# Performance work log

Measured on AMD Instinct MI355X. Metric: run time of the kernel, lower is better.

Reference implementation:

```python
import jax, jax.numpy as jnp
import numpy as np

B, FIN, FOUT, FH2, NMIX, LAT, H, W = 16, 256, 256, 256, 8, 512, 64, 64


def _xavier(key, shape):
    # xavier_normal_ over last-two-ish dims; simple fan-based scale
    fan_in = int(np.prod(shape[1:]))
    fan_out = shape[0]
    s = (2.0 / (fan_in + fan_out)) ** 0.5
    return jax.random.normal(key, shape, jnp.float32) * s


def setup_inputs() -> dict:
    key = jax.random.key(0)
    ks = jax.random.split(key, 12)
    return {
        "x": jax.random.normal(ks[0], (B, FIN, H, W), jnp.float32),
        "lat": jax.random.normal(ks[1], (B, LAT), jnp.float32),
        # mixture kernel banks [n_mix, out_ch, in_ch] (kernel_size=1 squeezed)
        "k_in_mix": _xavier(ks[2], (NMIX, FH2, FIN)),
        "k_mid_mix": _xavier(ks[3], (NMIX, FH2, 2 * FH2)),
        "k_out_mix": _xavier(ks[4], (NMIX, FOUT, 2 * FH2)),
        "k_short_mix": _xavier(ks[5], (NMIX, FOUT, FIN)),
        # mixture bias banks [n_mix, ch]
        "b_in_mix": _xavier(ks[6], (NMIX, FH2)),
        "b_mid_mix": _xavier(ks[7], (NMIX, FH2)),
        "b_out_mix": _xavier(ks[8], (NMIX, FOUT)),
        "b_short_mix": _xavier(ks[9], (NMIX, FOUT)),
        # dyna_mix = nn.Linear(lat_size, n_mix) (lat_factor=0 path)
        "w_dyna": _xavier(ks[10], (NMIX, LAT)),
        "b_dyna": jnp.zeros((NMIX,), jnp.float32),
    }


def _complex_wave(h):
    # doubles channel dim: concat(sin, cos) along channels (per sample)
    return jnp.concatenate([jnp.sin(h), jnp.cos(h)], axis=1)


def reference(x, lat, k_in_mix, k_mid_mix, k_out_mix, k_short_mix,
              b_in_mix, b_mid_mix, b_out_mix, b_short_mix, w_dyna, b_dyna):
    # mixing coefficients per sample: [B, n_mix]
    mix = lat @ w_dyna.T + b_dyna
    # per-sample 1x1 conv kernels via mixture reduction: [B, out, in]
    k_in = jnp.einsum('bm,moi->boi', mix, k_in_mix)
    k_mid = jnp.einsum('bm,moi->boi', mix, k_mid_mix)
    k_out = jnp.einsum('bm,moi->boi', mix, k_out_mix)
    k_short = jnp.einsum('bm,moi->boi', mix, k_short_mix)
    # per-sample biases: [B, ch, 1, 1]
    b_in = (mix @ b_in_mix)[:, :, None, None]
    b_mid = (mix @ b_mid_mix)[:, :, None, None]
    b_out = (mix @ b_out_mix)[:, :, None, None]
    b_short = (mix @ b_short_mix)[:, :, None, None]
    # grouped conv with groups = batch (kernel_size=1) == per-sample matmul
    short = jnp.einsum('boi,bihw->bohw', k_short, x) + b_short
    h = jnp.einsum('boi,bihw->bohw', k_in, x) + b_in            # [B, FH2, H, W]
    h = _complex_wave(h)                                        # [B, 2*FH2, H, W]
    h = jnp.einsum('boi,bihw->bohw', k_mid, h) + b_mid
    h = _complex_wave(h)
    out = jnp.einsum('boi,bihw->bohw', k_out, h) + b_out + short
    return out
```

## Files before the change

kernel.cpp:

```cpp
#include <hip/hip_runtime.h>
#include <stdint.h>

#define B_    16
#define FIN   256
#define FOUT  256
#define FH2   256
#define NMIX  8
#define LAT   512
#define HW    4096
#define MT    32

typedef short bf16x8 __attribute__((ext_vector_type(8)));
typedef float f32x4  __attribute__((ext_vector_type(4)));

#define WS_MIX    0
#define WS_BIAS   1024
#define WS_WIN    131072
#define WS_WMID   2228224
#define WS_WOUT   6422528
#define WS_WSHORT 10616832

__device__ __forceinline__ uint16_t f2bf(float f) {
  uint32_t u = __builtin_bit_cast(uint32_t, f);
  u += 0x7fffu + ((u >> 16) & 1u);
  return (uint16_t)(u >> 16);
}
__device__ __forceinline__ uint32_t pack2(float lo, float hi) {
  return (uint32_t)f2bf(lo) | ((uint32_t)f2bf(hi) << 16);
}

#define MFMA(a, b, c) __builtin_amdgcn_mfma_f32_16x16x32_bf16(a, b, c, 0, 0, 0)

__global__ void k_mix_bias(const float* __restrict__ lat,
                           const float* __restrict__ w_dyna,
                           const float* __restrict__ b_dyna,
                           const float* __restrict__ b_in_mix,
                           const float* __restrict__ b_mid_mix,
                           const float* __restrict__ b_out_mix,
                           const float* __restrict__ b_short_mix,
                           float* __restrict__ ws_mix,
                           float* __restrict__ ws_bias) {
  __shared__ float smix[NMIX];
  const int t = threadIdx.x;
  const int lane = t & 63, wv = t >> 6;
  const int b = blockIdx.x;
#pragma unroll
  for (int d2 = 0; d2 < 2; d2++) {
    int m = wv * 2 + d2;
    float s = 0.f;
#pragma unroll
    for (int j = 0; j < 8; j++)
      s += lat[b * LAT + j * 64 + lane] * w_dyna[m * LAT + j * 64 + lane];
#pragma unroll
    for (int off = 32; off; off >>= 1) s += __shfl_xor(s, off);
    if (lane == 0) {
      float v = s + b_dyna[m];
      ws_mix[b * NMIX + m] = v;
      smix[m] = v;
    }
  }
  __syncthreads();
  const float* banks[4] = {b_in_mix, b_mid_mix, b_out_mix, b_short_mix};
  for (int pos = t; pos < 1024; pos += 256) {
    int bank = pos >> 8, ch = pos & 255;
    const float* bp = banks[bank];
    float a = 0.f;
#pragma unroll
    for (int m = 0; m < NMIX; m++) a += smix[m] * bp[m * 256 + ch];
    ws_bias[(bank * B_ + b) * 256 + ch] = a;
  }
}

__global__ void k_weights(const float* __restrict__ k_in_mix,
                          const float* __restrict__ k_mid_mix,
                          const float* __restrict__ k_out_mix,
                          const float* __restrict__ k_short_mix,
                          const float* __restrict__ ws_mix,
                          uint16_t* __restrict__ w_in,
                          uint16_t* __restrict__ w_mid,
                          uint16_t* __restrict__ w_out,
                          uint16_t* __restrict__ w_short) {
  __shared__ float smix[B_ * NMIX];
  const int t = threadIdx.x;
  if (t < B_ * NMIX) smix[t] = ws_mix[t];
  __syncthreads();
  const int idx = blockIdx.x * 256 + t;
  const float* src;
  uint16_t* dst;
  int sstride, dstride;
  if (idx < 65536) {
    int e = idx;
    int j = e & 7, lane = (e >> 3) & 63, ots = (e >> 9) & 3, kt = (e >> 11) & 7, wv = e >> 14;
    int row = wv * 64 + ots * 16 + (lane & 15);
    int k = kt * 32 + (lane >> 4) * 8 + j;
    src = k_in_mix + row * 256 + k; sstride = 65536;
    dst = w_in + e;                 dstride = 65536;
  } else if (idx < 196608) {
    int e = idx - 65536;
    int j = e & 7, lane = (e >> 3) & 63, ots = (e >> 9) & 3, kt = (e >> 11) & 15, wv = e >> 15;
    int row = wv * 64 + ots * 16 + (lane & 15);
    int kp = kt * 32 + (lane >> 4) * 8 + j;
    int i = (kp >> 1) + ((kp & 1) << 8);
    src = k_mid_mix + row * 512 + i; sstride = 131072;
    dst = w_mid + e;                 dstride = 131072;
  } else if (idx < 327680) {
    int e = idx - 196608;
    int j = e & 7, lane = (e >> 3) & 63, ots = (e >> 9) & 3, kt = (e >> 11) & 15, wv = e >> 15;
    int row = wv * 64 + ots * 16 + (lane & 15);
    int kp = kt * 32 + (lane >> 4) * 8 + j;
    int i = (kp >> 1) + ((kp & 1) << 8);
    src = k_out_mix + row * 512 + i; sstride = 131072;
    dst = w_out + e;                 dstride = 131072;
  } else {
    int e = idx - 327680;
    int j = e & 7, lane = (e >> 3) & 63, ots = (e >> 9) & 3, kt = (e >> 11) & 7, wv = e >> 14;
    int row = wv * 64 + ots * 16 + (lane & 15);
    int k = kt * 32 + (lane >> 4) * 8 + j;
    src = k_short_mix + row * 256 + k; sstride = 65536;
    dst = w_short + e;                 dstride = 65536;
  }
  float v[NMIX];
#pragma unroll
  for (int m = 0; m < NMIX; m++) v[m] = src[m * sstride];
  for (int b = 0; b < B_; b++) {
    float a = 0.f;
#pragma unroll
    for (int m = 0; m < NMIX; m++) a += smix[b * NMIX + m] * v[m];
    dst[b * dstride] = f2bf(a);
  }
}

__launch_bounds__(256, 3)
__global__ void k_main(const float* __restrict__ x,
                       const float* __restrict__ ws_bias,
                       const uint16_t* __restrict__ w_in,
                       const uint16_t* __restrict__ w_mid,
                       const uint16_t* __restrict__ w_out,
                       const uint16_t* __restrict__ w_short,
                       float* __restrict__ out) {
  __shared__ int4 smem4[49152 / 16];
  char* lds = (char*)smem4;
  char* Xb = lds;
  char* H1 = lds + 16384;
  char* H2 = lds;

  const int t = threadIdx.x;
  const int lane = t & 63;
  const int wv = t >> 6;
  const int q = lane >> 4;
  const int n = lane & 15;
  const int b = blockIdx.x & 15;
  const int p0 = (blockIdx.x >> 4) * MT;

  {
    const float* xb = x + (size_t)b * FIN * HW + p0;
    const int p = t & 31;
    const int cg = t >> 5;
#pragma unroll
    for (int cc = 0; cc < 4; cc++) {
      int c = cg * 4 + cc;
      float v[8];
#pragma unroll
      for (int e = 0; e < 8; e++) v[e] = xb[(size_t)(c * 8 + e) * HW + p];
      int4 pkt = make_int4((int)pack2(v[0], v[1]), (int)pack2(v[2], v[3]),
                           (int)pack2(v[4], v[5]), (int)pack2(v[6], v[7]));
      *(int4*)(Xb + p * 512 + ((c ^ (p & 7)) * 16)) = pkt;
    }
  }
  __syncthreads();

  f32x4 acc_h[4][2], acc_s[4][2];
#pragma unroll
  for (int ots = 0; ots < 4; ots++) {
    int o = wv * 64 + ots * 16 + q * 4;
    float4 vi = *(const float4*)&ws_bias[(0 * B_ + b) * 256 + o];
    float4 vs = *(const float4*)&ws_bias[(3 * B_ + b) * 256 + o];
    acc_h[ots][0][0] = vi.x; acc_h[ots][0][1] = vi.y; acc_h[ots][0][2] = vi.z; acc_h[ots][0][3] = vi.w;
    acc_h[ots][1] = acc_h[ots][0];
    acc_s[ots][0][0] = vs.x; acc_s[ots][0][1] = vs.y; acc_s[ots][0][2] = vs.z; acc_s[ots][0][3] = vs.w;
    acc_s[ots][1] = acc_s[ots][0];
  }
  {
    const uint16_t* Wi = w_in + (size_t)b * 65536 + wv * 16384 + lane * 8;
    const uint16_t* Ws = w_short + (size_t)b * 65536 + wv * 16384 + lane * 8;
#pragma unroll
    for (int kt = 0; kt < 8; kt++) {
      int sw = ((kt * 4 + q) ^ (n & 7)) * 16;
      bf16x8 bf0 = *(const bf16x8*)(Xb + n * 512 + sw);
      bf16x8 bf1 = *(const bf16x8*)(Xb + (16 + n) * 512 + sw);
#pragma unroll
      for (int ots = 0; ots < 4; ots++) {
        bf16x8 ai = *(const bf16x8*)(Wi + kt * 2048 + ots * 512);
        bf16x8 as = *(const bf16x8*)(Ws + kt * 2048 + ots * 512);
        acc_h[ots][0] = MFMA(ai, bf0, acc_h[ots][0]);
        acc_h[ots][1] = MFMA(ai, bf1, acc_h[ots][1]);
        acc_s[ots][0] = MFMA(as, bf0, acc_s[ots][0]);
        acc_s[ots][1] = MFMA(as, bf1, acc_s[ots][1]);
      }
    }
  }
#pragma unroll
  for (int ots = 0; ots < 4; ots++) {
    int ctile = (wv * 4 + ots) * 4 + q;
#pragma unroll
    for (int pt = 0; pt < 2; pt++) {
      int p = pt * 16 + n;
      uint32_t u0 = pack2(__sinf(acc_h[ots][pt][0]), __cosf(acc_h[ots][pt][0]));
      uint32_t u1 = pack2(__sinf(acc_h[ots][pt][1]), __cosf(acc_h[ots][pt][1]));
      uint32_t u2 = pack2(__sinf(acc_h[ots][pt][2]), __cosf(acc_h[ots][pt][2]));
      uint32_t u3 = pack2(__sinf(acc_h[ots][pt][3]), __cosf(acc_h[ots][pt][3]));
      *(int4*)(H1 + p * 1024 + ((ctile ^ (p & 7)) * 16)) =
          make_int4((int)u0, (int)u1, (int)u2, (int)u3);
    }
  }
  __syncthreads();

  f32x4 acc2[4][2];
#pragma unroll
  for (int ots = 0; ots < 4; ots++) {
    int o = wv * 64 + ots * 16 + q * 4;
    float4 v = *(const float4*)&ws_bias[(1 * B_ + b) * 256 + o];
    acc2[ots][0][0] = v.x; acc2[ots][0][1] = v.y; acc2[ots][0][2] = v.z; acc2[ots][0][3] = v.w;
    acc2[ots][1] = acc2[ots][0];
  }
  {
    const uint16_t* Wm = w_mid + (size_t)b * 131072 + wv * 32768 + lane * 8;
#pragma unroll
    for (int kt = 0; kt < 16; kt++) {
      int sw = ((kt * 4 + q) ^ (n & 7)) * 16;
      bf16x8 bf0 = *(const bf16x8*)(H1 + n * 1024 + sw);
      bf16x8 bf1 = *(const bf16x8*)(H1 + (16 + n) * 1024 + sw);
#pragma unroll
      for (int ots = 0; ots < 4; ots++) {
        bf16x8 am = *(const bf16x8*)(Wm + kt * 2048 + ots * 512);
        acc2[ots][0] = MFMA(am, bf0, acc2[ots][0]);
        acc2[ots][1] = MFMA(am, bf1, acc2[ots][1]);
      }
    }
  }
  __syncthreads();
#pragma unroll
  for (int ots = 0; ots < 4; ots++) {
    int ctile = (wv * 4 + ots) * 4 + q;
#pragma unroll
    for (int pt = 0; pt < 2; pt++) {
      int p = pt * 16 + n;
      uint32_t u0 = pack2(__sinf(acc2[ots][pt][0]), __cosf(acc2[ots][pt][0]));
      uint32_t u1 = pack2(__sinf(acc2[ots][pt][1]), __cosf(acc2[ots][pt][1]));
      uint32_t u2 = pack2(__sinf(acc2[ots][pt][2]), __cosf(acc2[ots][pt][2]));
      uint32_t u3 = pack2(__sinf(acc2[ots][pt][3]), __cosf(acc2[ots][pt][3]));
      *(int4*)(H2 + p * 1024 + ((ctile ^ (p & 7)) * 16)) =
          make_int4((int)u0, (int)u1, (int)u2, (int)u3);
    }
  }
  __syncthreads();

  f32x4 acc3[4][2];
#pragma unroll
  for (int ots = 0; ots < 4; ots++) {
    int o = wv * 64 + ots * 16 + q * 4;
    float4 v = *(const float4*)&ws_bias[(2 * B_ + b) * 256 + o];
    acc3[ots][0][0] = acc_s[ots][0][0] + v.x; acc3[ots][0][1] = acc_s[ots][0][1] + v.y;
    acc3[ots][0][2] = acc_s[ots][0][2] + v.z; acc3[ots][0][3] = acc_s[ots][0][3] + v.w;
    acc3[ots][1][0] = acc_s[ots][1][0] + v.x; acc3[ots][1][1] = acc_s[ots][1][1] + v.y;
    acc3[ots][1][2] = acc_s[ots][1][2] + v.z; acc3[ots][1][3] = acc_s[ots][1][3] + v.w;
  }
  {
    const uint16_t* Wo = w_out + (size_t)b * 131072 + wv * 32768 + lane * 8;
#pragma unroll
    for (int kt = 0; kt < 16; kt++) {
      int sw = ((kt * 4 + q) ^ (n & 7)) * 16;
      bf16x8 bf0 = *(const bf16x8*)(H2 + n * 1024 + sw);
      bf16x8 bf1 = *(const bf16x8*)(H2 + (16 + n) * 1024 + sw);
#pragma unroll
      for (int ots = 0; ots < 4; ots++) {
        bf16x8 ao = *(const bf16x8*)(Wo + kt * 2048 + ots * 512);
        acc3[ots][0] = MFMA(ao, bf0, acc3[ots][0]);
        acc3[ots][1] = MFMA(ao, bf1, acc3[ots][1]);
      }
    }
  }
  {
    float* ob = out + (size_t)b * FOUT * HW + p0;
#pragma unroll
    for (int ots = 0; ots < 4; ots++) {
#pragma unroll
      for (int pt = 0; pt < 2; pt++) {
#pragma unroll
        for (int r = 0; r < 4; r++) {
          int o = wv * 64 + ots * 16 + q * 4 + r;
          ob[(size_t)o * HW + pt * 16 + n] = acc3[ots][pt][r];
        }
      }
    }
  }
}

extern "C" void kernel_launch(void* const* d_in, const int* in_sizes, int n_in,
                              void* d_out, int out_size, void* d_ws, size_t ws_size,
                              hipStream_t stream) {
  const float* x           = (const float*)d_in[0];
  const float* lat         = (const float*)d_in[1];
  const float* k_in_mix    = (const float*)d_in[2];
  const float* k_mid_mix   = (const float*)d_in[3];
  const float* k_out_mix   = (const float*)d_in[4];
  const float* k_short_mix = (const float*)d_in[5];
  const float* b_in_mix    = (const float*)d_in[6];
  const float* b_mid_mix   = (const float*)d_in[7];
  const float* b_out_mix   = (const float*)d_in[8];
  const float* b_short_mix = (const float*)d_in[9];
  const float* w_dyna      = (const float*)d_in[10];
  const float* b_dyna      = (const float*)d_in[11];

  char* ws = (char*)d_ws;
  float*    ws_mix  = (float*)(ws + WS_MIX);
  float*    ws_bias = (float*)(ws + WS_BIAS);
  uint16_t* w_in    = (uint16_t*)(ws + WS_WIN);
  uint16_t* w_mid   = (uint16_t*)(ws + WS_WMID);
  uint16_t* w_out   = (uint16_t*)(ws + WS_WOUT);
  uint16_t* w_short = (uint16_t*)(ws + WS_WSHORT);
  float* out = (float*)d_out;

  hipLaunchKernelGGL(k_mix_bias, dim3(16), dim3(256), 0, stream,
                     lat, w_dyna, b_dyna, b_in_mix, b_mid_mix, b_out_mix,
                     b_short_mix, ws_mix, ws_bias);
  hipLaunchKernelGGL(k_weights, dim3(1536), dim3(256), 0, stream,
                     k_in_mix, k_mid_mix, k_out_mix, k_short_mix, ws_mix,
                     w_in, w_mid, w_out, w_short);
  hipLaunchKernelGGL(k_main, dim3(2048), dim3(256), 0, stream,
                     x, ws_bias, w_in, w_mid, w_out, w_short, out);
}
```

Measured before the change: 232.5 us.

## Double pixel tile and software-pipeline weight and input loads across K

Doubles the pixel tile per block from 32 to 64, which halves the grid. Each weight fragment loaded from global memory now feeds four MFMA columns instead of two. The first layer streams x in K-chunks through a double-buffered LDS slab, overlapping the next chunk's global load with the current MFMAs. The mid and out layers prefetch weights two steps ahead with a triple-register buffer. The short-path accumulator is reused as the output accumulator. LDS grows to 72KB and accumulator registers double, so occupancy drops to 2 blocks per CU, which risks spills and less latency hiding.

```diff
diff --git a/kernel.cpp b/kernel.cpp
--- a/kernel.cpp
+++ b/kernel.cpp
@@ -8,7 +8,7 @@
 #define NMIX  8
 #define LAT   512
 #define HW    4096
-#define MT    32
+#define MT    64
 
 typedef short bf16x8 __attribute__((ext_vector_type(8)));
 typedef float f32x4  __attribute__((ext_vector_type(4)));
@@ -130,7 +130,7 @@
   }
 }
 
-__launch_bounds__(256, 3)
+__launch_bounds__(256, 2)
 __global__ void k_main(const float* __restrict__ x,
                        const float* __restrict__ ws_bias,
                        const uint16_t* __restrict__ w_in,
@@ -138,11 +138,10 @@
                        const uint16_t* __restrict__ w_out,
                        const uint16_t* __restrict__ w_short,
                        float* __restrict__ out) {
-  __shared__ int4 smem4[49152 / 16];
+  __shared__ int4 smem4[73728 / 16];
   char* lds = (char*)smem4;
-  char* Xb = lds;
-  char* H1 = lds + 16384;
-  char* H2 = lds;
+  char* Xc = lds;
+  char* H1 = lds + 8192;
 
   const int t = threadIdx.x;
   const int lane = t & 63;
@@ -152,144 +151,196 @@
   const int b = blockIdx.x & 15;
   const int p0 = (blockIdx.x >> 4) * MT;
 
+  const float* xb = x + (size_t)b * FIN * HW + p0;
+  const int xpos = t & 63;
+  const int xcg = wv;
+
   {
-    const float* xb = x + (size_t)b * FIN * HW + p0;
-    const int p = t & 31;
-    const int cg = t >> 5;
-#pragma unroll
-    for (int cc = 0; cc < 4; cc++) {
-      int c = cg * 4 + cc;
-      float v[8];
-#pragma unroll
-      for (int e = 0; e < 8; e++) v[e] = xb[(size_t)(c * 8 + e) * HW + p];
-      int4 pkt = make_int4((int)pack2(v[0], v[1]), (int)pack2(v[2], v[3]),
-                           (int)pack2(v[4], v[5]), (int)pack2(v[6], v[7]));
-      *(int4*)(Xb + p * 512 + ((c ^ (p & 7)) * 16)) = pkt;
-    }
-  }
-  __syncthreads();
-
-  f32x4 acc_h[4][2], acc_s[4][2];
-#pragma unroll
-  for (int ots = 0; ots < 4; ots++) {
-    int o = wv * 64 + ots * 16 + q * 4;
-    float4 vi = *(const float4*)&ws_bias[(0 * B_ + b) * 256 + o];
-    float4 vs = *(const float4*)&ws_bias[(3 * B_ + b) * 256 + o];
-    acc_h[ots][0][0] = vi.x; acc_h[ots][0][1] = vi.y; acc_h[ots][0][2] = vi.z; acc_h[ots][0][3] = vi.w;
-    acc_h[ots][1] = acc_h[ots][0];
-    acc_s[ots][0][0] = vs.x; acc_s[ots][0][1] = vs.y; acc_s[ots][0][2] = vs.z; acc_s[ots][0][3] = vs.w;
-    acc_s[ots][1] = acc_s[ots][0];
-  }
-  {
-    const uint16_t* Wi = w_in + (size_t)b * 65536 + wv * 16384 + lane * 8;
-    const uint16_t* Ws = w_short + (size_t)b * 65536 + wv * 16384 + lane * 8;
-#pragma unroll
-    for (int kt = 0; kt < 8; kt++) {
-      int sw = ((kt * 4 + q) ^ (n & 7)) * 16;
-      bf16x8 bf0 = *(const bf16x8*)(Xb + n * 512 + sw);
-      bf16x8 bf1 = *(const bf16x8*)(Xb + (16 + n) * 512 + sw);
+    const float* xs = xb + (size_t)(xcg * 8) * HW + xpos;
+    float v[8];
+#pragma unroll
+    for (int e = 0; e < 8; e++) v[e] = xs[(size_t)e * HW];
+    *(int4*)(Xc + xpos * 64 + ((xcg ^ (xpos & 3)) * 16)) =
+        make_int4((int)pack2(v[0], v[1]), (int)pack2(v[2], v[3]),
+                  (int)pack2(v[4], v[5]), (int)pack2(v[6], v[7]));
+  }
+
+  f32x4 acc_h[4][4], acc_s[4][4];
+#pragma unroll
+  for (int ots = 0; ots < 4; ots++) {
+    const int o = wv * 64 + ots * 16 + q * 4;
+    const float4 vi = *(const float4*)&ws_bias[(0 * B_ + b) * 256 + o];
+    const float4 vs = *(const float4*)&ws_bias[(3 * B_ + b) * 256 + o];
+    f32x4 ah, asv;
+    ah[0] = vi.x; ah[1] = vi.y; ah[2] = vi.z; ah[3] = vi.w;
+    asv[0] = vs.x; asv[1] = vs.y; asv[2] = vs.z; asv[3] = vs.w;
+#pragma unroll
+    for (int pt = 0; pt < 4; pt++) { acc_h[ots][pt] = ah; acc_s[ots][pt] = asv; }
+  }
+
+  const uint16_t* Wi = w_in + (size_t)b * 65536 + wv * 16384 + lane * 8;
+  const uint16_t* Ws = w_short + (size_t)b * 65536 + wv * 16384 + lane * 8;
+  bf16x8 ai[2][4], asf[2][4];
+#pragma unroll
+  for (int ots = 0; ots < 4; ots++) {
+    ai[0][ots] = *(const bf16x8*)(Wi + ots * 512);
+    asf[0][ots] = *(const bf16x8*)(Ws + ots * 512);
+  }
+  __syncthreads();
+
+#pragma unroll
+  for (int kt = 0; kt < 8; kt++) {
+    float xv[8];
+    if (kt < 7) {
+      const float* xs = xb + (size_t)((kt + 1) * 32 + xcg * 8) * HW + xpos;
+#pragma unroll
+      for (int e = 0; e < 8; e++) xv[e] = xs[(size_t)e * HW];
 #pragma unroll
       for (int ots = 0; ots < 4; ots++) {
-        bf16x8 ai = *(const bf16x8*)(Wi + kt * 2048 + ots * 512);
-        bf16x8 as = *(const bf16x8*)(Ws + kt * 2048 + ots * 512);
-        acc_h[ots][0] = MFMA(ai, bf0, acc_h[ots][0]);
-        acc_h[ots][1] = MFMA(ai, bf1, acc_h[ots][1]);
-        acc_s[ots][0] = MFMA(as, bf0, acc_s[ots][0]);
-        acc_s[ots][1] = MFMA(as, bf1, acc_s[ots][1]);
+        ai[(kt + 1) & 1][ots] = *(const bf16x8*)(Wi + (kt + 1) * 2048 + ots * 512);
+        asf[(kt + 1) & 1][ots] = *(const bf16x8*)(Ws + (kt + 1) * 2048 + ots * 512);
       }
     }
-  }
-#pragma unroll
-  for (int ots = 0; ots < 4; ots++) {
-    int ctile = (wv * 4 + ots) * 4 + q;
-#pragma unroll
-    for (int pt = 0; pt < 2; pt++) {
-      int p = pt * 16 + n;
-      uint32_t u0 = pack2(__sinf(acc_h[ots][pt][0]), __cosf(acc_h[ots][pt][0]));
-      uint32_t u1 = pack2(__sinf(acc_h[ots][pt][1]), __cosf(acc_h[ots][pt][1]));
-      uint32_t u2 = pack2(__sinf(acc_h[ots][pt][2]), __cosf(acc_h[ots][pt][2]));
-      uint32_t u3 = pack2(__sinf(acc_h[ots][pt][3]), __cosf(acc_h[ots][pt][3]));
-      *(int4*)(H1 + p * 1024 + ((ctile ^ (p & 7)) * 16)) =
-          make_int4((int)u0, (int)u1, (int)u2, (int)u3);
-    }
-  }
-  __syncthreads();
-
-  f32x4 acc2[4][2];
-#pragma unroll
-  for (int ots = 0; ots < 4; ots++) {
-    int o = wv * 64 + ots * 16 + q * 4;
-    float4 v = *(const float4*)&ws_bias[(1 * B_ + b) * 256 + o];
-    acc2[ots][0][0] = v.x; acc2[ots][0][1] = v.y; acc2[ots][0][2] = v.z; acc2[ots][0][3] = v.w;
-    acc2[ots][1] = acc2[ots][0];
-  }
-  {
-    const uint16_t* Wm = w_mid + (size_t)b * 131072 + wv * 32768 + lane * 8;
-#pragma unroll
-    for (int kt = 0; kt < 16; kt++) {
-      int sw = ((kt * 4 + q) ^ (n & 7)) * 16;
-      bf16x8 bf0 = *(const bf16x8*)(H1 + n * 1024 + sw);
-      bf16x8 bf1 = *(const bf16x8*)(H1 + (16 + n) * 1024 + sw);
-#pragma unroll
-      for (int ots = 0; ots < 4; ots++) {
-        bf16x8 am = *(const bf16x8*)(Wm + kt * 2048 + ots * 512);
-        acc2[ots][0] = MFMA(am, bf0, acc2[ots][0]);
-        acc2[ots][1] = MFMA(am, bf1, acc2[ots][1]);
+    const char* Xr = Xc + (kt & 1) * 4096;
+    bf16x8 bf[4];
+#pragma unroll
+    for (int pt = 0; pt < 4; pt++) {
+      const int p = pt * 16 + n;
+      bf[pt] = *(const bf16x8*)(Xr + p * 64 + ((q ^ (p & 3)) * 16));
+    }
+#pragma unroll
+    for (int ots = 0; ots < 4; ots++) {
+#pragma unroll
+      for (int pt = 0; pt < 4; pt++) {
+        acc_h[ots][pt] = MFMA(ai[kt & 1][ots], bf[pt], acc_h[ots][pt]);
+        acc_s[ots][pt] = MFMA(asf[kt & 1][ots], bf[pt], acc_s[ots][pt]);
       }
     }
-  }
-  __syncthreads();
-#pragma unroll
-  for (int ots = 0; ots < 4; ots++) {
-    int ctile = (wv * 4 + ots) * 4 + q;
-#pragma unroll
-    for (int pt = 0; pt < 2; pt++) {
-      int p = pt * 16 + n;
-      uint32_t u0 = pack2(__sinf(acc2[ots][pt][0]), __cosf(acc2[ots][pt][0]));
-      uint32_t u1 = pack2(__sinf(acc2[ots][pt][1]), __cosf(acc2[ots][pt][1]));
-      uint32_t u2 = pack2(__sinf(acc2[ots][pt][2]), __cosf(acc2[ots][pt][2]));
-      uint32_t u3 = pack2(__sinf(acc2[ots][pt][3]), __cosf(acc2[ots][pt][3]));
-      *(int4*)(H2 + p * 1024 + ((ctile ^ (p & 7)) * 16)) =
-          make_int4((int)u0, (int)u1, (int)u2, (int)u3);
-    }
-  }
-  __syncthreads();
-
-  f32x4 acc3[4][2];
-#pragma unroll
-  for (int ots = 0; ots < 4; ots++) {
-    int o = wv * 64 + ots * 16 + q * 4;
-    float4 v = *(const float4*)&ws_bias[(2 * B_ + b) * 256 + o];
-    acc3[ots][0][0] = acc_s[ots][0][0] + v.x; acc3[ots][0][1] = acc_s[ots][0][1] + v.y;
-    acc3[ots][0][2] = acc_s[ots][0][2] + v.z; acc3[ots][0][3] = acc_s[ots][0][3] + v.w;
-    acc3[ots][1][0] = acc_s[ots][1][0] + v.x; acc3[ots][1][1] = acc_s[ots][1][1] + v.y;
-    acc3[ots][1][2] = acc_s[ots][1][2] + v.z; acc3[ots][1][3] = acc_s[ots][1][3] + v.w;
-  }
-  {
-    const uint16_t* Wo = w_out + (size_t)b * 131072 + wv * 32768 + lane * 8;
-#pragma unroll
-    for (int kt = 0; kt < 16; kt++) {
-      int sw = ((kt * 4 + q) ^ (n & 7)) * 16;
-      bf16x8 bf0 = *(const bf16x8*)(H2 + n * 1024 + sw);
-      bf16x8 bf1 = *(const bf16x8*)(H2 + (16 + n) * 1024 + sw);
-#pragma unroll
-      for (int ots = 0; ots < 4; ots++) {
-        bf16x8 ao = *(const bf16x8*)(Wo + kt * 2048 + ots * 512);
-        acc3[ots][0] = MFMA(ao, bf0, acc3[ots][0]);
-        acc3[ots][1] = MFMA(ao, bf1, acc3[ots][1]);
-      }
-    }
-  }
+    if (kt < 7) {
+      *(int4*)(Xc + ((kt + 1) & 1) * 4096 + xpos * 64 + ((xcg ^ (xpos & 3)) * 16)) =
+          make_int4((int)pack2(xv[0], xv[1]), (int)pack2(xv[2], xv[3]),
+                    (int)pack2(xv[4], xv[5]), (int)pack2(xv[6], xv[7]));
+      __syncthreads();
+    }
+  }
+
+#pragma unroll
+  for (int ots = 0; ots < 4; ots++) {
+    const int ctile = (wv * 4 + ots) * 4 + q;
+#pragma unroll
+    for (int pt = 0; pt < 4; pt++) {
+      const int p = pt * 16 + n;
+      *(int4*)(H1 + p * 1024 + ((ctile ^ (p & 7)) * 16)) = make_int4(
+          (int)pack2(__sinf(acc_h[ots][pt][0]), __cosf(acc_h[ots][pt][0])),
+          (int)pack2(__sinf(acc_h[ots][pt][1]), __cosf(acc_h[ots][pt][1])),
+          (int)pack2(__sinf(acc_h[ots][pt][2]), __cosf(acc_h[ots][pt][2])),
+          (int)pack2(__sinf(acc_h[ots][pt][3]), __cosf(acc_h[ots][pt][3])));
+    }
+  }
+
+  const uint16_t* Wm = w_mid + (size_t)b * 131072 + wv * 32768 + lane * 8;
+  bf16x8 am[3][4];
+#pragma unroll
+  for (int ots = 0; ots < 4; ots++) {
+    am[0][ots] = *(const bf16x8*)(Wm + ots * 512);
+    am[1][ots] = *(const bf16x8*)(Wm + 2048 + ots * 512);
+  }
+  f32x4 acc2[4][4];
+#pragma unroll
+  for (int ots = 0; ots < 4; ots++) {
+    const int o = wv * 64 + ots * 16 + q * 4;
+    const float4 v = *(const float4*)&ws_bias[(1 * B_ + b) * 256 + o];
+    f32x4 a2;
+    a2[0] = v.x; a2[1] = v.y; a2[2] = v.z; a2[3] = v.w;
+#pragma unroll
+    for (int pt = 0; pt < 4; pt++) acc2[ots][pt] = a2;
+  }
+  __syncthreads();
+
+#pragma unroll
+  for (int kt = 0; kt < 16; kt++) {
+    if (kt < 14) {
+#pragma unroll
+      for (int ots = 0; ots < 4; ots++)
+        am[(kt + 2) % 3][ots] = *(const bf16x8*)(Wm + (kt + 2) * 2048 + ots * 512);
+    }
+    bf16x8 bf[4];
+#pragma unroll
+    for (int pt = 0; pt < 4; pt++) {
+      const int p = pt * 16 + n;
+      bf[pt] = *(const bf16x8*)(H1 + p * 1024 + (((kt * 4 + q) ^ (p & 7)) * 16));
+    }
+#pragma unroll
+    for (int ots = 0; ots < 4; ots++)
+#pragma unroll
+      for (int pt = 0; pt < 4; pt++)
+        acc2[ots][pt] = MFMA(am[kt % 3][ots], bf[pt], acc2[ots][pt]);
+  }
+  __syncthreads();
+
+#pragma unroll
+  for (int ots = 0; ots < 4; ots++) {
+    const int ctile = (wv * 4 + ots) * 4 + q;
+#pragma unroll
+    for (int pt = 0; pt < 4; pt++) {
+      const int p = pt * 16 + n;
+      *(int4*)(H1 + p * 1024 + ((ctile ^ (p & 7)) * 16)) = make_int4(
+          (int)pack2(__sinf(acc2[ots][pt][0]), __cosf(acc2[ots][pt][0])),
+          (int)pack2(__sinf(acc2[ots][pt][1]), __cosf(acc2[ots][pt][1])),
+          (int)pack2(__sinf(acc2[ots][pt][2]), __cosf(acc2[ots][pt][2])),
+          (int)pack2(__sinf(acc2[ots][pt][3]), __cosf(acc2[ots][pt][3])));
+    }
+  }
+
+  const uint16_t* Wo = w_out + (size_t)b * 131072 + wv * 32768 + lane * 8;
+  bf16x8 ao[3][4];
+#pragma unroll
+  for (int ots = 0; ots < 4; ots++) {
+    ao[0][ots] = *(const bf16x8*)(Wo + ots * 512);
+    ao[1][ots] = *(const bf16x8*)(Wo + 2048 + ots * 512);
+  }
+#pragma unroll
+  for (int ots = 0; ots < 4; ots++) {
+    const int o = wv * 64 + ots * 16 + q * 4;
+    const float4 v = *(const float4*)&ws_bias[(2 * B_ + b) * 256 + o];
+#pragma unroll
+    for (int pt = 0; pt < 4; pt++) {
+      acc_s[ots][pt][0] += v.x; acc_s[ots][pt][1] += v.y;
+      acc_s[ots][pt][2] += v.z; acc_s[ots][pt][3] += v.w;
+    }
+  }
+  __syncthreads();
+
+#pragma unroll
+  for (int kt = 0; kt < 16; kt++) {
+    if (kt < 14) {
+#pragma unroll
+      for (int ots = 0; ots < 4; ots++)
+        ao[(kt + 2) % 3][ots] = *(const bf16x8*)(Wo + (kt + 2) * 2048 + ots * 512);
+    }
+    bf16x8 bf[4];
+#pragma unroll
+    for (int pt = 0; pt < 4; pt++) {
+      const int p = pt * 16 + n;
+      bf[pt] = *(const bf16x8*)(H1 + p * 1024 + (((kt * 4 + q) ^ (p & 7)) * 16));
+    }
+#pragma unroll
+    for (int ots = 0; ots < 4; ots++)
+#pragma unroll
+      for (int pt = 0; pt < 4; pt++)
+        acc_s[ots][pt] = MFMA(ao[kt % 3][ots], bf[pt], acc_s[ots][pt]);
+  }
+
   {
     float* ob = out + (size_t)b * FOUT * HW + p0;
 #pragma unroll
     for (int ots = 0; ots < 4; ots++) {
 #pragma unroll
-      for (int pt = 0; pt < 2; pt++) {
+      for (int pt = 0; pt < 4; pt++) {
 #pragma unroll
         for (int r = 0; r < 4; r++) {
-          int o = wv * 64 + ots * 16 + q * 4 + r;
-          ob[(size_t)o * HW + pt * 16 + n] = acc3[ots][pt][r];
+          const int o = wv * 64 + ots * 16 + q * 4 + r;
+          ob[(size_t)o * HW + pt * 16 + n] = acc_s[ots][pt][r];
         }
       }
     }
@@ -327,6 +378,6 @@
   hipLaunchKernelGGL(k_weights, dim3(1536), dim3(256), 0, stream,
                      k_in_mix, k_mid_mix, k_out_mix, k_short_mix, ws_mix,
                      w_in, w_mid, w_out, w_short);
-  hipLaunchKernelGGL(k_main, dim3(2048), dim3(256), 0, stream,
+  hipLaunchKernelGGL(k_main, dim3(1024), dim3(256), 0, stream,
                      x, ws_bias, w_in, w_mid, w_out, w_short, out);
 }
```

New measurement: 207.5 us. 1.12x faster.
